# Optimization experiments

Hardware: AMD Instinct MI355X
Metric: run time of the kernel (lower is better)

Reference implementation:

```python
import jax, jax.numpy as jnp
import numpy as np

B, S, D_MODEL, D_HEAD = 8, 2048, 1024, 128
MAX_ROUNDS = 3
THRESH = 0.1
SCALE = 1.0 / np.sqrt(float(D_HEAD))


def setup_inputs() -> dict:
    key = jax.random.key(0)
    ks = jax.random.split(key, 12)

    def lin(k, out_d, in_d):
        # torch Linear weight layout [out, in], y = x @ W.T + b
        return (jax.random.normal(k, (out_d, in_d), jnp.float32) / np.sqrt(float(in_d))).astype(jnp.float32)

    thesis_w = lin(ks[3], D_HEAD, D_HEAD)
    return {
        "x": jax.random.normal(ks[0], (B, S, D_MODEL), jnp.float32),
        "wq": lin(ks[1], D_HEAD, D_MODEL),
        "wk": lin(ks[2], D_HEAD, D_MODEL),
        "wv": lin(ks[4], D_HEAD, D_MODEL),
        "thesis_w": thesis_w,  # antithesis weight is -thesis_w per __init__
        "thesis_b": 0.02 * jax.random.normal(ks[5], (D_HEAD,), jnp.float32),
        "anti_b": 0.02 * jax.random.normal(ks[6], (D_HEAD,), jnp.float32),
        "s_w1": lin(ks[7], D_HEAD, 3 * D_HEAD),
        "s_b1": jnp.zeros((D_HEAD,), jnp.float32),
        "s_w2": lin(ks[8], D_HEAD, D_HEAD),
        "s_b2": jnp.zeros((D_HEAD,), jnp.float32),
        "g_w": lin(ks[9], 1, 2 * D_HEAD),
        "g_b": jnp.zeros((1,), jnp.float32),
    }


def reference(x, wq, wk, wv, thesis_w, thesis_b, anti_b, s_w1, s_b1, s_w2, s_b2, g_w, g_b):
    # q/k/v projections (no bias)
    q = jnp.einsum("bsm,hm->bsh", x, wq)
    k = jnp.einsum("bsm,hm->bsh", x, wk)
    v = jnp.einsum("bsm,hm->bsh", x, wv)

    attn = jax.nn.softmax(jnp.einsum("bqh,bkh->bqk", q, k) * SCALE, axis=-1)
    # dropout is identity at eval time
    cur = jnp.einsum("bqk,bkh->bqh", attn, v)  # [B,S,Dh]

    # attn_weights and v never change across rounds, so thesis/antithesis are
    # round-invariant: compute the context projections once.
    context = cur
    thesis = context @ thesis_w.T + thesis_b
    anti = context @ (-thesis_w).T + anti_b  # antithesis weight = -thesis weight

    active = jnp.ones((B, S), dtype=bool)
    for _ in range(MAX_ROUNDS):
        # emulate `if not active_mask.any(): break` under jit
        any_active = jnp.any(active)
        am = active[..., None].astype(x.dtype)
        at, aa, ac = thesis * am, anti * am, cur * am

        h = jax.nn.relu(jnp.concatenate([at, aa, ac], axis=-1) @ s_w1.T + s_b1)
        synth = h @ s_w2.T + s_b2
        gate = jax.nn.sigmoid(jnp.concatenate([ac, synth], axis=-1) @ g_w.T + g_b)
        update = gate * (synth - ac) * 0.1
        new = cur + update  # applied to ALL tokens, matching original

        stable = jnp.linalg.norm(update, axis=-1) < THRESH  # new - cur == update
        cur = jnp.where(any_active, new, cur)
        active = jnp.where(any_active, active & ~stable, active)
    return cur
```

## Files before the change

### kernel.cpp

```cpp
#include <hip/hip_runtime.h>
#include <hip/hip_bf16.h>

#define B_   8
#define S_   2048
#define DM   1024
#define DH   128
#define BS_  16384
#define SCALE_  0.08838834764831845f
#define SCALE2_ 0.12751744f

typedef unsigned short u16;
typedef unsigned int   u32;
typedef _Float16 half8 __attribute__((ext_vector_type(8)));
typedef float    f32x4 __attribute__((ext_vector_type(4)));
typedef u32      u32x4 __attribute__((ext_vector_type(4)));

union H8 { u32x4 v; u32 u[4]; half8 h; };

__device__ __forceinline__ float bf2f(u16 u) {
    union { u32 i; float f; } w; w.i = ((u32)u) << 16; return w.f;
}
__device__ __forceinline__ void unpack8(uint4 v, float* f) {
    f[0] = bf2f(v.x & 0xffff); f[1] = bf2f(v.x >> 16);
    f[2] = bf2f(v.y & 0xffff); f[3] = bf2f(v.y >> 16);
    f[4] = bf2f(v.z & 0xffff); f[5] = bf2f(v.z >> 16);
    f[6] = bf2f(v.w & 0xffff); f[7] = bf2f(v.w >> 16);
}
__device__ __forceinline__ float ldE(const void* b, size_t i, int isbf16) {
    return isbf16 ? bf2f(((const u16*)b)[i]) : ((const float*)b)[i];
}
__device__ __forceinline__ void ld8(const void* b, size_t i, int isbf16, float* f) {
    if (isbf16) {
        unpack8(*(const uint4*)((const u16*)b + i), f);
    } else {
        float4 a = *(const float4*)((const float*)b + i);
        float4 c = *(const float4*)((const float*)b + i + 4);
        f[0] = a.x; f[1] = a.y; f[2] = a.z; f[3] = a.w;
        f[4] = c.x; f[5] = c.y; f[6] = c.z; f[7] = c.w;
    }
}
__device__ __forceinline__ u32 f2pk(float v) {
    _Float16 h = (_Float16)v;
    _Float16 l = (_Float16)(v - (float)h);
    union { _Float16 f; u16 u; } a, b; a.f = h; b.f = l;
    return ((u32)a.u << 16) | (u32)b.u;
}
__device__ __forceinline__ void split8(const float* f, u32x4& hi, u32x4& lo) {
    u32 H[8], L[8];
#pragma unroll
    for (int j = 0; j < 8; ++j) {
        _Float16 h = (_Float16)f[j];
        _Float16 l = (_Float16)(f[j] - (float)h);
        union { _Float16 x; u16 u; } a, b; a.x = h; b.x = l;
        H[j] = a.u; L[j] = b.u;
    }
    hi = (u32x4){H[0] | (H[1] << 16), H[2] | (H[3] << 16), H[4] | (H[5] << 16), H[6] | (H[7] << 16)};
    lo = (u32x4){L[0] | (L[1] << 16), L[2] | (L[3] << 16), L[4] | (L[5] << 16), L[6] | (L[7] << 16)};
}
__device__ __forceinline__ u32 permHI(u32 eB, u32 eA) { return __builtin_amdgcn_perm(eB, eA, 0x07060302u); }
__device__ __forceinline__ u32 permLO(u32 eB, u32 eA) { return __builtin_amdgcn_perm(eB, eA, 0x05040100u); }
__device__ __forceinline__ u16 f2h(float v) { union { _Float16 f; u16 u; } a; a.f = (_Float16)v; return a.u; }
__device__ __forceinline__ float h2f(u16 u) { union { _Float16 f; u16 u; } a; a.u = u; return (float)a.f; }

__global__ void init_kernel(const void* x, int* flag, int* active, int* counts) {
    int i = blockIdx.x * 256 + threadIdx.x;
    if (i < BS_) active[i] = 1;
    if (i < 4) counts[i] = (i == 0) ? BS_ : 0;
    if (i == 0) {
        const u16* w = (const u16*)x;
        int sane = 0;
        for (int t = 0; t < 256; ++t) {
            int e = (w[2 * t] >> 7) & 0xFF;
            if (e >= 100 && e <= 135) ++sane;
        }
        *flag = (sane >= 192) ? 1 : 0;
    }
}

__global__ __launch_bounds__(256) void prepack_w_kernel(
    const void* __restrict__ wq, const void* __restrict__ wk, const void* __restrict__ wv,
    const int* __restrict__ flag, u32x4* __restrict__ wpk)
{
    const int isb = *flag;
    const int gid = blockIdx.x * 256 + threadIdx.x;
    const int l  = gid & 63;
    const int t  = (gid >> 6) & 7;
    const int ks = (gid >> 9) & 31;
    const int z  = gid >> 14;
    const void* W = (z == 0) ? wq : (z == 1) ? wk : wv;
    const int row = 16 * t + (l & 15);
    const int k0  = ks * 32 + 8 * (l >> 4);
    float f[8];
    ld8(W, (size_t)row * DM + k0, isb, f);
    u32x4 hi, lo;
    split8(f, hi, lo);
    const size_t base = ((((size_t)z * 32 + ks) * 16) + 2 * t) * 64 + l;
    wpk[base]      = hi;
    wpk[base + 64] = lo;
}

__global__ __launch_bounds__(256) void qkv_kernel(
    const void* __restrict__ x, const u32x4* __restrict__ wpk,
    const int* __restrict__ flag, u32* __restrict__ qkv)
{
    const int isb = *flag;
    const int z = blockIdx.z;
    u32* out = qkv + (size_t)z * ((size_t)BS_ * DH);
    const int bx = blockIdx.x;
    const int m0 = ((bx & 7) * 32 + (bx >> 3)) * 64;
    const int tid = threadIdx.x;
    const int wave = tid >> 6, lane = tid & 63;
    const int qd = lane >> 4, c = lane & 15;

    __shared__ u32x4 WL[2][8][2][64];

    const u32x4* wz = wpk + (size_t)z * (32 * 16 * 64);
    const size_t arow = (size_t)(m0 + wave * 16 + c) * DM + 8 * qd;

#define STAGE_W(ks_, b_)                                                          \
    {                                                                             \
        const u32x4* _src = wz + ((size_t)(ks_) * 16 + 4 * wave) * 64 + lane;     \
        _Pragma("unroll")                                                         \
        for (int _j = 0; _j < 4; ++_j) {                                          \
            __builtin_amdgcn_global_load_lds(                                     \
                (const __attribute__((address_space(1))) u32*)(_src + _j * 64),   \
                (__attribute__((address_space(3))) u32*)&WL[b_][2 * wave + (_j >> 1)][_j & 1][0], \
                16, 0, 0);                                                        \
        }                                                                         \
    }

    float Ar[8], Arn[8];
    ld8(x, arow, isb, Ar);
    STAGE_W(0, 0);
    ld8(x, arow + 32, isb, Arn);
    __syncthreads();

    f32x4 acc[8] = {};

    for (int ks = 0; ks < 32; ++ks) {
        const int cb = ks & 1;
        if (ks + 1 < 32) STAGE_W(ks + 1, cb ^ 1);

        H8 Ah, Al;
        split8(Ar, Ah.v, Al.v);
#pragma unroll
        for (int t = 0; t < 8; ++t) {
            H8 bh, bl;
            bh.v = WL[cb][t][0][lane]; bl.v = WL[cb][t][1][lane];
            acc[t] = __builtin_amdgcn_mfma_f32_16x16x32_f16(Al.h, bh.h, acc[t], 0, 0, 0);
            acc[t] = __builtin_amdgcn_mfma_f32_16x16x32_f16(Ah.h, bl.h, acc[t], 0, 0, 0);
            acc[t] = __builtin_amdgcn_mfma_f32_16x16x32_f16(Ah.h, bh.h, acc[t], 0, 0, 0);
        }
#pragma unroll
        for (int j = 0; j < 8; ++j) Ar[j] = Arn[j];
        if (ks + 2 < 32) ld8(x, arow + (size_t)(ks + 2) * 32, isb, Arn);
        __syncthreads();
    }
#undef STAGE_W

#pragma unroll
    for (int r = 0; r < 4; ++r) {
        const int row = m0 + wave * 16 + qd * 4 + r;
        u32* op = out + (size_t)row * DH + c;
#pragma unroll
        for (int t = 0; t < 8; ++t) op[t * 16] = f2pk(acc[t][r]);
    }
}

template <bool WRITE_PARTIAL>
__device__ __forceinline__ void attn_body(
    const u32* qp, const u32* __restrict__ kp, const u32* __restrict__ vp,
    u16* outO, u16* outL, float* cur,
    int b, int q0, int kt0, int kt1, int part)
{
    const int tid = threadIdx.x;
    const int wave = tid >> 6, lane = tid & 63;
    const int qd = lane >> 4, c = lane & 15;

    __shared__ u32x4 KF[2][2][4][64];
    __shared__ u32x4 VF[2][8][64];
    __shared__ u16   PB[4][531];

    H8 Qh[4];
    {
        const u32* qr = qp + ((size_t)b * S_ + q0 + wave * 16 + c) * DH;
#pragma unroll
        for (int ks = 0; ks < 4; ++ks) {
            uint4 e0 = *(const uint4*)(qr + ks * 32 + qd * 8);
            uint4 e1 = *(const uint4*)(qr + ks * 32 + qd * 8 + 4);
            Qh[ks].u[0] = permHI(e0.y, e0.x); Qh[ks].u[1] = permHI(e0.w, e0.z);
            Qh[ks].u[2] = permHI(e1.y, e1.x); Qh[ks].u[3] = permHI(e1.w, e1.z);
        }
    }

    const int kKey = tid & 31, kD0 = (tid >> 5) * 16;
    const int vD = tid >> 1, vKg = (tid & 1) * 16;
    const int tK = (tid >> 4) & 1, cK = tid & 15;
    const int tV = tid >> 5,      cV = (tid >> 1) & 15;

    uint4 Kst[4]; u32 Vst[16];

    auto loadKV = [&](int kb) {
        const u32* kr = kp + ((size_t)b * S_ + kb * 32 + kKey) * DH + kD0;
#pragma unroll
        for (int j = 0; j < 4; ++j) Kst[j] = *(const uint4*)(kr + 4 * j);
        const u32* vc = vp + ((size_t)b * S_ + kb * 32 + vKg) * DH + vD;
#pragma unroll
        for (int j = 0; j < 16; ++j) Vst[j] = vc[(size_t)j * DH];
    };
    auto writeKV = [&](int wb) {
#pragma unroll
        for (int g = 0; g < 2; ++g) {
            const int dg = kD0 + 8 * g, ksK = dg >> 5, qK = (dg >> 3) & 3;
            KF[wb][tK][ksK][qK * 16 + cK] = (u32x4){
                permHI(Kst[2*g].y, Kst[2*g].x), permHI(Kst[2*g].w, Kst[2*g].z),
                permHI(Kst[2*g+1].y, Kst[2*g+1].x), permHI(Kst[2*g+1].w, Kst[2*g+1].z)};
        }
#pragma unroll
        for (int g = 0; g < 2; ++g) {
            const int qV = 2 * (tid & 1) + g;
            VF[wb][tV][qV * 16 + cV] = (u32x4){
                permHI(Vst[8*g+1], Vst[8*g+0]), permHI(Vst[8*g+3], Vst[8*g+2]),
                permHI(Vst[8*g+5], Vst[8*g+4]), permHI(Vst[8*g+7], Vst[8*g+6])};
        }
    };

    loadKV(kt0);
    writeKV(0);
    if (kt0 + 1 < kt1) loadKV(kt0 + 1);
    __syncthreads();

    f32x4 O[8] = {};
    float lsum[4] = {};

    for (int kt = kt0; kt < kt1; ++kt) {
        const int cb = (kt - kt0) & 1;

        f32x4 S0 = {}, S1 = {};
#pragma unroll
        for (int ks = 0; ks < 4; ++ks) {
            H8 kh;
            kh.v = KF[cb][0][ks][lane];
            S0 = __builtin_amdgcn_mfma_f32_16x16x32_f16(Qh[ks].h, kh.h, S0, 0, 0, 0);
            kh.v = KF[cb][1][ks][lane];
            S1 = __builtin_amdgcn_mfma_f32_16x16x32_f16(Qh[ks].h, kh.h, S1, 0, 0, 0);
        }

        u16* pw = PB[wave];
#pragma unroll
        for (int r = 0; r < 4; ++r) {
            float e0 = exp2f(fmaf(S0[r], SCALE2_, -4.0f));
            float e1 = exp2f(fmaf(S1[r], SCALE2_, -4.0f));
            lsum[r] += e0 + e1;
            pw[(4 * qd + r) * 33 + c]      = f2h(e0);
            pw[(4 * qd + r) * 33 + 16 + c] = f2h(e1);
        }

        u16 e[8];
#pragma unroll
        for (int j = 0; j < 8; ++j) e[j] = pw[c * 33 + 8 * qd + j];
        H8 Ph;
        Ph.u[0] = (u32)e[0] | ((u32)e[1] << 16);
        Ph.u[1] = (u32)e[2] | ((u32)e[3] << 16);
        Ph.u[2] = (u32)e[4] | ((u32)e[5] << 16);
        Ph.u[3] = (u32)e[6] | ((u32)e[7] << 16);

#pragma unroll
        for (int t = 0; t < 8; ++t) {
            H8 vh;
            vh.v = VF[cb][t][lane];
            O[t] = __builtin_amdgcn_mfma_f32_16x16x32_f16(Ph.h, vh.h, O[t], 0, 0, 0);
        }

        if (kt + 1 < kt1) {
            writeKV((kt + 1 - kt0) & 1);
            if (kt + 2 < kt1) loadKV(kt + 2);
        }
        __syncthreads();
    }

    if (WRITE_PARTIAL) {
        float lred[4];
#pragma unroll
        for (int r = 0; r < 4; ++r) {
            float l = lsum[r];
            l += __shfl_xor(l, 1); l += __shfl_xor(l, 2);
            l += __shfl_xor(l, 4); l += __shfl_xor(l, 8);
            lred[r] = l;
        }
        const size_t rb = (size_t)b * S_ + q0 + wave * 16 + 4 * qd;
        u16* Op = outO + (size_t)part * ((size_t)BS_ * DH);
#pragma unroll
        for (int t = 0; t < 8; ++t)
#pragma unroll
            for (int r = 0; r < 4; ++r)
                Op[(rb + r) * DH + t * 16 + c] = f2h(O[t][r]);
        if (c == 0) {
            u16* lp = outL + (size_t)part * BS_;
#pragma unroll
            for (int r = 0; r < 4; ++r) lp[rb + r] = f2h(lred[r]);
        }
    } else {
        float linv[4];
#pragma unroll
        for (int r = 0; r < 4; ++r) {
            float l = lsum[r];
            l += __shfl_xor(l, 1); l += __shfl_xor(l, 2);
            l += __shfl_xor(l, 4); l += __shfl_xor(l, 8);
            linv[r] = 1.0f / l;
        }
        const size_t rb = (size_t)b * S_ + q0 + wave * 16 + 4 * qd;
#pragma unroll
        for (int t = 0; t < 8; ++t)
#pragma unroll
            for (int r = 0; r < 4; ++r)
                cur[(rb + r) * DH + t * 16 + c] = O[t][r] * linv[r];
    }
}

__global__ __launch_bounds__(256) void attn_kernel(
    const u32* qp, const u32* __restrict__ kp, const u32* __restrict__ vp, float* cur)
{
    const int rid = blockIdx.x + 32 * blockIdx.y;
    attn_body<false>(qp, kp, vp, nullptr, nullptr, cur,
                     rid & 7, ((rid >> 3) & 31) * 64, 0, S_ / 32, 0);
}

__global__ __launch_bounds__(256) void attn_split_kernel(
    const u32* qp, const u32* __restrict__ kp, const u32* __restrict__ vp,
    u16* __restrict__ Opart, u16* __restrict__ lpart)
{
    const int rid = blockIdx.x + 32 * (blockIdx.y + 8 * blockIdx.z);
    const int b    = rid & 7;
    const int qx   = (rid >> 3) & 31;
    const int part = rid >> 8;
    const int quart = S_ / 128;
    attn_body<true>(qp, kp, vp, Opart, lpart, nullptr,
                    b, qx * 64, part * quart, (part + 1) * quart, part);
}

__global__ __launch_bounds__(256) void combine_kernel(
    const u16* __restrict__ Opart, const u16* __restrict__ lpart,
    float* __restrict__ cur)
{
    const size_t N1 = (size_t)BS_ * DH;
    const size_t i0 = ((size_t)blockIdx.x * 256 + threadIdx.x) * 16;
    const int row = (int)(i0 >> 7);
    const float lt = h2f(lpart[row]) + h2f(lpart[BS_ + row])
                   + h2f(lpart[2 * BS_ + row]) + h2f(lpart[3 * BS_ + row]);
    const float linv = 1.0f / lt;
    float acc[16] = {};
#pragma unroll
    for (int p = 0; p < 4; ++p) {
        const u16* op = Opart + (size_t)p * N1 + i0;
        uint4 v0 = *(const uint4*)op;
        uint4 v1 = *(const uint4*)(op + 8);
        const u32 w[8] = {v0.x, v0.y, v0.z, v0.w, v1.x, v1.y, v1.z, v1.w};
#pragma unroll
        for (int j = 0; j < 8; ++j) {
            acc[2 * j]     += h2f((u16)(w[j] & 0xffff));
            acc[2 * j + 1] += h2f((u16)(w[j] >> 16));
        }
    }
#pragma unroll
    for (int t = 0; t < 4; ++t)
        *(float4*)(cur + i0 + t * 4) = make_float4(
            acc[4*t] * linv, acc[4*t+1] * linv, acc[4*t+2] * linv, acc[4*t+3] * linv);
}

__global__ __launch_bounds__(256) void prepack_rw_kernel(
    const void* __restrict__ tw, const void* __restrict__ w1, const void* __restrict__ w2,
    const int* __restrict__ flag, u32x4* __restrict__ pk)
{
    const int isb = *flag;
    const int gid = blockIdx.x * 256 + threadIdx.x;
    const int l = gid & 63, t = (gid >> 6) & 7, ks = (gid >> 9) & 3, mat = gid >> 11;
    const int row = 16 * t + (l & 15);
    const int k0  = ks * 32 + 8 * (l >> 4);
    float f[8];
    if (mat == 0)      ld8(tw, (size_t)row * DH + k0, isb, f);
    else if (mat <= 3) ld8(w1, (size_t)row * 384 + (mat - 1) * 128 + k0, isb, f);
    else               ld8(w2, (size_t)row * DH + k0, isb, f);
    u32x4 hi, lo;
    split8(f, hi, lo);
    const size_t base = (((size_t)mat * 4 + ks) * 16 + 2 * t) * 64 + l;
    pk[base] = hi; pk[base + 64] = lo;
}

struct Afrag { H8 h[4], l[4]; };
__device__ __forceinline__ void splitA(const float (&A)[4][8], Afrag& F) {
#pragma unroll
    for (int ks = 0; ks < 4; ++ks) split8(A[ks], F.h[ks].v, F.l[ks].v);
}
__device__ __forceinline__ void gemm_wb(const Afrag& F, const u32x4 (*WB)[16][64],
                                        const int lane, f32x4 (&acc)[8])
{
#pragma unroll
    for (int ks = 0; ks < 4; ++ks) {
#pragma unroll
        for (int t = 0; t < 8; ++t) {
            H8 bh, bl;
            bh.v = WB[ks][2 * t][lane];
            bl.v = WB[ks][2 * t + 1][lane];
            acc[t] = __builtin_amdgcn_mfma_f32_16x16x32_f16(F.l[ks].h, bh.h, acc[t], 0, 0, 0);
            acc[t] = __builtin_amdgcn_mfma_f32_16x16x32_f16(F.h[ks].h, bl.h, acc[t], 0, 0, 0);
            acc[t] = __builtin_amdgcn_mfma_f32_16x16x32_f16(F.h[ks].h, bh.h, acc[t], 0, 0, 0);
        }
    }
}

__global__ __launch_bounds__(256) void round_kernel(
    const float* cur0, const float* curr,
    const u32x4* __restrict__ pk,
    const void* __restrict__ tb, const void* __restrict__ ab,
    const void* __restrict__ b1, const void* __restrict__ b2,
    const void* __restrict__ gw, const void* __restrict__ gb,
    const int* __restrict__ flag, int* active, int* counts, int r,
    float* cur_out, void* dout)
{
    const int isb = *flag;
    const int tok0 = blockIdx.x * 64;
    const int tid = threadIdx.x;
    const bool last = (dout != nullptr);

    if (counts[r] <= 0) {
        if (last) {
            for (int e = tid; e < 64 * DH; e += 256) {
                size_t idx = (size_t)tok0 * DH + e;
                float v = curr[idx];
                if (isb) ((__hip_bfloat16*)dout)[idx] = __float2bfloat16(v);
                else     ((float*)dout)[idx] = v;
            }
        }
        return;
    }

    const int wave = tid >> 6, lane = tid & 63;
    const int qd = lane >> 4, c = lane & 15;

    __shared__ u32x4 WB[4][16][64];
    __shared__ float T0S[64][132];
    __shared__ float HSS[64][132];
    __shared__ float actS[64], tbS[128], abS[128], b1S[128], b2S[128], gwS[256];
    __shared__ int blkcnt;

#define STAGE_RW(mat_)                                                             \
    {                                                                              \
        _Pragma("unroll")                                                          \
        for (int _j = 0; _j < 16; ++_j) {                                          \
            __builtin_amdgcn_global_load_lds(                                      \
                (const __attribute__((address_space(1))) u32*)(                    \
                    pk + (((size_t)(mat_) * 4 + wave) * 16 + _j) * 64 + lane),     \
                (__attribute__((address_space(3))) u32*)&WB[wave][_j][0],          \
                16, 0, 0);                                                         \
        }                                                                          \
    }

    STAGE_RW(0);
    if (tid < 64) actS[tid] = active[tok0 + tid] ? 1.0f : 0.0f;
    if (tid < 128) {
        tbS[tid] = ldE(tb, tid, isb); abS[tid] = ldE(ab, tid, isb);
        b1S[tid] = ldE(b1, tid, isb); b2S[tid] = ldE(b2, tid, isb);
    }
    gwS[tid] = ldE(gw, tid, isb);
    if (tid == 0) blkcnt = 0;
    const float gbf = ldE(gb, 0, isb);

    const int rowl = 16 * wave + c;
    const int hr   = 16 * wave + 4 * qd;

    float A1[4][8];
    {
        const float* cr = cur0 + (size_t)(tok0 + rowl) * DH;
#pragma unroll
        for (int ks = 0; ks < 4; ++ks) {
            *(float4*)&A1[ks][0] = *(const float4*)(cr + ks * 32 + 8 * qd);
            *(float4*)&A1[ks][4] = *(const float4*)(cr + ks * 32 + 8 * qd + 4);
        }
    }
    Afrag FA; splitA(A1, FA);
    __syncthreads();

    {
        f32x4 acc[8] = {};
        gemm_wb(FA, WB, lane, acc);
#pragma unroll
        for (int t = 0; t < 8; ++t)
#pragma unroll
            for (int rr = 0; rr < 4; ++rr)
                T0S[hr + rr][16 * t + c] = acc[t][rr];
    }
    __syncthreads();
    STAGE_RW(1);

    f32x4 acc1[8] = {};
    const float am_r = actS[rowl];
    {
        float Ac[4][8];
#pragma unroll
        for (int ks = 0; ks < 4; ++ks)
#pragma unroll
            for (int j = 0; j < 8; ++j) {
                const int k = ks * 32 + 8 * qd + j;
                Ac[ks][j] = (T0S[rowl][k] + tbS[k]) * am_r;
            }
        Afrag FC; splitA(Ac, FC);
        __syncthreads();
        gemm_wb(FC, WB, lane, acc1);
    }
    __syncthreads();
    STAGE_RW(2);
    {
        float Ac[4][8];
#pragma unroll
        for (int ks = 0; ks < 4; ++ks)
#pragma unroll
            for (int j = 0; j < 8; ++j) {
                const int k = ks * 32 + 8 * qd + j;
                Ac[ks][j] = (abS[k] - T0S[rowl][k]) * am_r;
            }
        Afrag FC; splitA(Ac, FC);
        __syncthreads();
        gemm_wb(FC, WB, lane, acc1);
    }
    __syncthreads();
    STAGE_RW(3);
    {
        float Ac[4][8];
        const float* cr = curr + (size_t)(tok0 + rowl) * DH;
#pragma unroll
        for (int ks = 0; ks < 4; ++ks) {
            float4 a0 = *(const float4*)(cr + ks * 32 + 8 * qd);
            float4 a1 = *(const float4*)(cr + ks * 32 + 8 * qd + 4);
            Ac[ks][0] = a0.x * am_r; Ac[ks][1] = a0.y * am_r;
            Ac[ks][2] = a0.z * am_r; Ac[ks][3] = a0.w * am_r;
            Ac[ks][4] = a1.x * am_r; Ac[ks][5] = a1.y * am_r;
            Ac[ks][6] = a1.z * am_r; Ac[ks][7] = a1.w * am_r;
        }
        Afrag FC; splitA(Ac, FC);
        __syncthreads();
        gemm_wb(FC, WB, lane, acc1);
    }
#pragma unroll
    for (int t = 0; t < 8; ++t)
#pragma unroll
        for (int rr = 0; rr < 4; ++rr)
            HSS[hr + rr][16 * t + c] = fmaxf(acc1[t][rr] + b1S[16 * t + c], 0.0f);
    __syncthreads();
    STAGE_RW(4);
    {
        float Ac[4][8];
#pragma unroll
        for (int ks = 0; ks < 4; ++ks) {
            const float* hp = &HSS[rowl][ks * 32 + 8 * qd];
            *(float4*)&Ac[ks][0] = *(const float4*)hp;
            *(float4*)&Ac[ks][4] = *(const float4*)(hp + 4);
        }
        Afrag FC; splitA(Ac, FC);
        __syncthreads();
        f32x4 acc2[8] = {};
        gemm_wb(FC, WB, lane, acc2);
#pragma unroll
        for (int t = 0; t < 8; ++t)
#pragma unroll
            for (int rr = 0; rr < 4; ++rr)
                T0S[hr + rr][16 * t + c] = acc2[t][rr] + b2S[16 * t + c];
    }
    __syncthreads();

    const int tok = tid >> 2, d0 = (tid & 3) * 32;
    const float am = actS[tok];
    const float* cp = curr + (size_t)(tok0 + tok) * DH + d0;
    float cv[32];
#pragma unroll
    for (int t = 0; t < 8; ++t) {
        float4 vv = *(const float4*)(cp + t * 4);
        cv[t * 4] = vv.x; cv[t * 4 + 1] = vv.y; cv[t * 4 + 2] = vv.z; cv[t * 4 + 3] = vv.w;
    }
    const float* srow = &T0S[tok][d0];
    float gp = 0.0f;
#pragma unroll
    for (int e = 0; e < 32; ++e)
        gp += cv[e] * am * gwS[d0 + e] + srow[e] * gwS[128 + d0 + e];
    gp += __shfl_xor(gp, 1, 4);
    gp += __shfl_xor(gp, 2, 4);
    const float gate = 1.0f / (1.0f + __expf(-(gp + gbf)));
    float ss = 0.0f; float up[32];
#pragma unroll
    for (int e = 0; e < 32; ++e) {
        float u = gate * (srow[e] - cv[e] * am) * 0.1f;
        up[e] = u; ss += u * u;
    }
    ss += __shfl_xor(ss, 1, 4);
    ss += __shfl_xor(ss, 2, 4);
    const bool stable = sqrtf(ss) < 0.1f;

    if (last) {
        size_t off = (size_t)(tok0 + tok) * DH + d0;
        if (isb) {
            __hip_bfloat16* op = (__hip_bfloat16*)dout + off;
#pragma unroll
            for (int e = 0; e < 32; ++e) op[e] = __float2bfloat16(cv[e] + up[e]);
        } else {
            float* op = (float*)dout + off;
#pragma unroll
            for (int t = 0; t < 8; ++t)
                *(float4*)(op + t * 4) = make_float4(cv[t * 4] + up[t * 4], cv[t * 4 + 1] + up[t * 4 + 1],
                                                     cv[t * 4 + 2] + up[t * 4 + 2], cv[t * 4 + 3] + up[t * 4 + 3]);
        }
    } else {
        float* op = cur_out + (size_t)(tok0 + tok) * DH + d0;
#pragma unroll
        for (int t = 0; t < 8; ++t)
            *(float4*)(op + t * 4) = make_float4(cv[t * 4] + up[t * 4], cv[t * 4 + 1] + up[t * 4 + 1],
                                                 cv[t * 4 + 2] + up[t * 4 + 2], cv[t * 4 + 3] + up[t * 4 + 3]);
    }
    const int newact = (am > 0.0f && !stable) ? 1 : 0;
    if ((tid & 3) == 0) {
        active[tok0 + tok] = newact;
        if (newact) atomicAdd(&blkcnt, 1);
    }
    __syncthreads();
    if (tid == 0 && blkcnt > 0) atomicAdd(&counts[r + 1], blkcnt);
#undef STAGE_RW
}

extern "C" void kernel_launch(void* const* d_in, const int* in_sizes, int n_in,
                              void* d_out, int out_size, void* d_ws, size_t ws_size,
                              hipStream_t stream) {
    const void* x  = d_in[0];
    const void* wq = d_in[1];
    const void* wk = d_in[2];
    const void* wv = d_in[3];
    const void* tw = d_in[4];
    const void* tb = d_in[5];
    const void* ab = d_in[6];
    const void* w1 = d_in[7];
    const void* b1 = d_in[8];
    const void* w2 = d_in[9];
    const void* b2 = d_in[10];
    const void* gw = d_in[11];
    const void* gb = d_in[12];

    u32* ws = (u32*)d_ws;
    const size_t N1 = (size_t)BS_ * DH;
    u32* qp = ws;
    u32* kp = ws + N1;
    u32* vp = ws + 2 * N1;
    int* active = (int*)(ws + 3 * N1);
    int* counts = active + BS_;
    int* flag   = counts + 4;
    float* cur0  = (float*)qp;
    float* cur_r = (float*)kp;
    u16* Opart16 = (u16*)(ws + 3 * N1 + 32768);
    u16* lpart16 = (u16*)(ws + 5 * N1 + 32768);
    const bool big_ws = ws_size >= (size_t)42300000;
    u32x4* wpk = (u32x4*)(ws + 3 * N1 + 32768);
    u32x4* pkRW = (u32x4*)vp;

    init_kernel<<<dim3(BS_ / 256), 256, 0, stream>>>(x, flag, active, counts);
    prepack_w_kernel<<<dim3(192), 256, 0, stream>>>(wq, wk, wv, flag, wpk);
    qkv_kernel<<<dim3(BS_ / 64, 1, 3), 256, 0, stream>>>(x, wpk, flag, qp);
    if (big_ws) {
        attn_split_kernel<<<dim3(S_ / 64, B_, 4), 256, 0, stream>>>(qp, kp, vp, Opart16, lpart16);
        combine_kernel<<<dim3(512), 256, 0, stream>>>(Opart16, lpart16, cur0);
    } else {
        attn_kernel<<<dim3(S_ / 64, B_), 256, 0, stream>>>(qp, kp, vp, cur0);
    }
    prepack_rw_kernel<<<dim3(40), 256, 0, stream>>>(tw, w1, w2, flag, pkRW);
    round_kernel<<<dim3(BS_ / 64), 256, 0, stream>>>(
        cur0, cur0, pkRW, tb, ab, b1, b2, gw, gb, flag, active, counts, 0, cur_r, nullptr);
    round_kernel<<<dim3(BS_ / 64), 256, 0, stream>>>(
        cur0, cur_r, pkRW, tb, ab, b1, b2, gw, gb, flag, active, counts, 1, cur_r, nullptr);
    round_kernel<<<dim3(BS_ / 64), 256, 0, stream>>>(
        cur0, cur_r, pkRW, tb, ab, b1, b2, gw, gb, flag, active, counts, 2, cur_r, d_out);
}
```

Measured before the change: 283.6 us.

## Emit K/V in MFMA fragment layout and drop split-precision terms for bf16 inputs

The QKV kernel now writes K and V as half-precision MFMA-ready fragments, staged through shared memory, so the attention kernel reads them straight from global memory with no LDS staging, double buffering or per-tile barriers. When inputs are detected as bf16, the QKV GEMM uses only the high fp16 part, one MFMA instead of three, and the round kernel skips the hi*lo correction term. This cuts MFMA work and LDS traffic but lowers precision for K/V (fp16 only) and, on the bf16 path, for the projections. Attention now relies on cache behaviour instead of explicit LDS reuse.

```diff
diff --git a/kernel.cpp b/kernel.cpp
--- a/kernel.cpp
+++ b/kernel.cpp
@@ -57,8 +57,16 @@
     hi = (u32x4){H[0] | (H[1] << 16), H[2] | (H[3] << 16), H[4] | (H[5] << 16), H[6] | (H[7] << 16)};
     lo = (u32x4){L[0] | (L[1] << 16), L[2] | (L[3] << 16), L[4] | (L[5] << 16), L[6] | (L[7] << 16)};
 }
+__device__ __forceinline__ void cvt8hi(const float* f, u32x4& hi) {
+    u32 H[8];
+#pragma unroll
+    for (int j = 0; j < 8; ++j) {
+        union { _Float16 x; u16 u; } a; a.x = (_Float16)f[j];
+        H[j] = a.u;
+    }
+    hi = (u32x4){H[0] | (H[1] << 16), H[2] | (H[3] << 16), H[4] | (H[5] << 16), H[6] | (H[7] << 16)};
+}
 __device__ __forceinline__ u32 permHI(u32 eB, u32 eA) { return __builtin_amdgcn_perm(eB, eA, 0x07060302u); }
-__device__ __forceinline__ u32 permLO(u32 eB, u32 eA) { return __builtin_amdgcn_perm(eB, eA, 0x05040100u); }
 __device__ __forceinline__ u16 f2h(float v) { union { _Float16 f; u16 u; } a; a.f = (_Float16)v; return a.u; }
 __device__ __forceinline__ float h2f(u16 u) { union { _Float16 f; u16 u; } a; a.u = u; return (float)a.f; }
 
@@ -101,11 +109,11 @@
 
 __global__ __launch_bounds__(256) void qkv_kernel(
     const void* __restrict__ x, const u32x4* __restrict__ wpk,
-    const int* __restrict__ flag, u32* __restrict__ qkv)
+    const int* __restrict__ flag, u32* __restrict__ qout,
+    u32x4* __restrict__ kfrag, u32x4* __restrict__ vfrag)
 {
     const int isb = *flag;
     const int z = blockIdx.z;
-    u32* out = qkv + (size_t)z * ((size_t)BS_ * DH);
     const int bx = blockIdx.x;
     const int m0 = ((bx & 7) * 32 + (bx >> 3)) * 64;
     const int tid = threadIdx.x;
@@ -113,6 +121,7 @@
     const int qd = lane >> 4, c = lane & 15;
 
     __shared__ u32x4 WL[2][8][2][64];
+    __shared__ u16 TS[64][136];
 
     const u32x4* wz = wpk + (size_t)z * (32 * 16 * 64);
     const size_t arow = (size_t)(m0 + wave * 16 + c) * DM + 8 * qd;
@@ -141,15 +150,26 @@
         const int cb = ks & 1;
         if (ks + 1 < 32) STAGE_W(ks + 1, cb ^ 1);
 
-        H8 Ah, Al;
-        split8(Ar, Ah.v, Al.v);
-#pragma unroll
-        for (int t = 0; t < 8; ++t) {
-            H8 bh, bl;
-            bh.v = WL[cb][t][0][lane]; bl.v = WL[cb][t][1][lane];
-            acc[t] = __builtin_amdgcn_mfma_f32_16x16x32_f16(Al.h, bh.h, acc[t], 0, 0, 0);
-            acc[t] = __builtin_amdgcn_mfma_f32_16x16x32_f16(Ah.h, bl.h, acc[t], 0, 0, 0);
-            acc[t] = __builtin_amdgcn_mfma_f32_16x16x32_f16(Ah.h, bh.h, acc[t], 0, 0, 0);
+        if (isb) {
+            H8 Ah;
+            cvt8hi(Ar, Ah.v);
+#pragma unroll
+            for (int t = 0; t < 8; ++t) {
+                H8 bh;
+                bh.v = WL[cb][t][0][lane];
+                acc[t] = __builtin_amdgcn_mfma_f32_16x16x32_f16(Ah.h, bh.h, acc[t], 0, 0, 0);
+            }
+        } else {
+            H8 Ah, Al;
+            split8(Ar, Ah.v, Al.v);
+#pragma unroll
+            for (int t = 0; t < 8; ++t) {
+                H8 bh, bl;
+                bh.v = WL[cb][t][0][lane]; bl.v = WL[cb][t][1][lane];
+                acc[t] = __builtin_amdgcn_mfma_f32_16x16x32_f16(Al.h, bh.h, acc[t], 0, 0, 0);
+                acc[t] = __builtin_amdgcn_mfma_f32_16x16x32_f16(Ah.h, bl.h, acc[t], 0, 0, 0);
+                acc[t] = __builtin_amdgcn_mfma_f32_16x16x32_f16(Ah.h, bh.h, acc[t], 0, 0, 0);
+            }
         }
 #pragma unroll
         for (int j = 0; j < 8; ++j) Ar[j] = Arn[j];
@@ -158,18 +178,54 @@
     }
 #undef STAGE_W
 
-#pragma unroll
-    for (int r = 0; r < 4; ++r) {
-        const int row = m0 + wave * 16 + qd * 4 + r;
-        u32* op = out + (size_t)row * DH + c;
-#pragma unroll
-        for (int t = 0; t < 8; ++t) op[t * 16] = f2pk(acc[t][r]);
+    if (z == 0) {
+#pragma unroll
+        for (int r = 0; r < 4; ++r) {
+            const int row = m0 + wave * 16 + qd * 4 + r;
+            u32* op = qout + (size_t)row * DH + c;
+#pragma unroll
+            for (int t = 0; t < 8; ++t) op[t * 16] = f2pk(acc[t][r]);
+        }
+    } else {
+#pragma unroll
+        for (int t = 0; t < 8; ++t)
+#pragma unroll
+            for (int r = 0; r < 4; ++r)
+                TS[wave * 16 + qd * 4 + r][16 * t + c] = f2h(acc[t][r]);
+        __syncthreads();
+        if (z == 1) {
+#pragma unroll
+            for (int i = 0; i < 4; ++i) {
+                const int f = tid + 256 * i;
+                const int lf = f & 63, ks = (f >> 6) & 3, sub = f >> 8;
+                const int key = sub * 16 + (lf & 15);
+                const int d0  = ks * 32 + 8 * (lf >> 4);
+                u32 w[4];
+#pragma unroll
+                for (int q = 0; q < 4; ++q)
+                    w[q] = (u32)TS[key][d0 + 2 * q] | ((u32)TS[key][d0 + 2 * q + 1] << 16);
+                kfrag[((size_t)(m0 / 16 + sub) * 4 + ks) * 64 + lf] = (u32x4){w[0], w[1], w[2], w[3]};
+            }
+        } else {
+#pragma unroll
+            for (int i = 0; i < 4; ++i) {
+                const int f = tid + 256 * i;
+                const int lf = f & 63, t = (f >> 6) & 7, sub = f >> 9;
+                const int kb2 = sub * 32 + 8 * (lf >> 4);
+                const int dh  = 16 * t + (lf & 15);
+                u32 w[4];
+#pragma unroll
+                for (int q = 0; q < 4; ++q)
+                    w[q] = (u32)TS[kb2 + 2 * q][dh] | ((u32)TS[kb2 + 2 * q + 1][dh] << 16);
+                vfrag[((size_t)(m0 / 32 + sub) * 8 + t) * 64 + lf] = (u32x4){w[0], w[1], w[2], w[3]};
+            }
+        }
     }
 }
 
 template <bool WRITE_PARTIAL>
 __device__ __forceinline__ void attn_body(
-    const u32* qp, const u32* __restrict__ kp, const u32* __restrict__ vp,
+    const u32* qp, const u32x4* __restrict__ kfrag, const u32x4* __restrict__ vfrag,
     u16* outO, u16* outL, float* cur,
     int b, int q0, int kt0, int kt1, int part)
 {
@@ -177,9 +233,7 @@
     const int wave = tid >> 6, lane = tid & 63;
     const int qd = lane >> 4, c = lane & 15;
 
-    __shared__ u32x4 KF[2][2][4][64];
-    __shared__ u32x4 VF[2][8][64];
-    __shared__ u16   PB[4][531];
+    __shared__ u16 PB[4][531];
 
     H8 Qh[4];
     {
@@ -193,56 +247,23 @@
         }
     }
 
-    const int kKey = tid & 31, kD0 = (tid >> 5) * 16;
-    const int vD = tid >> 1, vKg = (tid & 1) * 16;
-    const int tK = (tid >> 4) & 1, cK = tid & 15;
-    const int tV = tid >> 5,      cV = (tid >> 1) & 15;
-
-    uint4 Kst[4]; u32 Vst[16];
-
-    auto loadKV = [&](int kb) {
-        const u32* kr = kp + ((size_t)b * S_ + kb * 32 + kKey) * DH + kD0;
-#pragma unroll
-        for (int j = 0; j < 4; ++j) Kst[j] = *(const uint4*)(kr + 4 * j);
-        const u32* vc = vp + ((size_t)b * S_ + kb * 32 + vKg) * DH + vD;
-#pragma unroll
-        for (int j = 0; j < 16; ++j) Vst[j] = vc[(size_t)j * DH];
-    };
-    auto writeKV = [&](int wb) {
-#pragma unroll
-        for (int g = 0; g < 2; ++g) {
-            const int dg = kD0 + 8 * g, ksK = dg >> 5, qK = (dg >> 3) & 3;
-            KF[wb][tK][ksK][qK * 16 + cK] = (u32x4){
-                permHI(Kst[2*g].y, Kst[2*g].x), permHI(Kst[2*g].w, Kst[2*g].z),
-                permHI(Kst[2*g+1].y, Kst[2*g+1].x), permHI(Kst[2*g+1].w, Kst[2*g+1].z)};
-        }
-#pragma unroll
-        for (int g = 0; g < 2; ++g) {
-            const int qV = 2 * (tid & 1) + g;
-            VF[wb][tV][qV * 16 + cV] = (u32x4){
-                permHI(Vst[8*g+1], Vst[8*g+0]), permHI(Vst[8*g+3], Vst[8*g+2]),
-                permHI(Vst[8*g+5], Vst[8*g+4]), permHI(Vst[8*g+7], Vst[8*g+6])};
-        }
-    };
-
-    loadKV(kt0);
-    writeKV(0);
-    if (kt0 + 1 < kt1) loadKV(kt0 + 1);
-    __syncthreads();
-
     f32x4 O[8] = {};
     float lsum[4] = {};
 
+    const u32x4* kb0 = kfrag + (size_t)b * 128 * 256;
+    const u32x4* vb0 = vfrag + (size_t)b * 64 * 512;
+
     for (int kt = kt0; kt < kt1; ++kt) {
-        const int cb = (kt - kt0) & 1;
+        const u32x4* kf = kb0 + (size_t)kt * 512;
+        const u32x4* vf = vb0 + (size_t)kt * 512;
 
         f32x4 S0 = {}, S1 = {};
 #pragma unroll
         for (int ks = 0; ks < 4; ++ks) {
             H8 kh;
-            kh.v = KF[cb][0][ks][lane];
+            kh.v = kf[ks * 64 + lane];
             S0 = __builtin_amdgcn_mfma_f32_16x16x32_f16(Qh[ks].h, kh.h, S0, 0, 0, 0);
-            kh.v = KF[cb][1][ks][lane];
+            kh.v = kf[256 + ks * 64 + lane];
             S1 = __builtin_amdgcn_mfma_f32_16x16x32_f16(Qh[ks].h, kh.h, S1, 0, 0, 0);
         }
 
@@ -268,15 +289,9 @@
 #pragma unroll
         for (int t = 0; t < 8; ++t) {
             H8 vh;
-            vh.v = VF[cb][t][lane];
+            vh.v = vf[t * 64 + lane];
             O[t] = __builtin_amdgcn_mfma_f32_16x16x32_f16(Ph.h, vh.h, O[t], 0, 0, 0);
         }
-
-        if (kt + 1 < kt1) {
-            writeKV((kt + 1 - kt0) & 1);
-            if (kt + 2 < kt1) loadKV(kt + 2);
-        }
-        __syncthreads();
     }
 
     if (WRITE_PARTIAL) {
@@ -319,15 +334,15 @@
 }
 
 __global__ __launch_bounds__(256) void attn_kernel(
-    const u32* qp, const u32* __restrict__ kp, const u32* __restrict__ vp, float* cur)
+    const u32* qp, const u32x4* __restrict__ kfrag, const u32x4* __restrict__ vfrag, float* cur)
 {
     const int rid = blockIdx.x + 32 * blockIdx.y;
-    attn_body<false>(qp, kp, vp, nullptr, nullptr, cur,
+    attn_body<false>(qp, kfrag, vfrag, nullptr, nullptr, cur,
                      rid & 7, ((rid >> 3) & 31) * 64, 0, S_ / 32, 0);
 }
 
 __global__ __launch_bounds__(256) void attn_split_kernel(
-    const u32* qp, const u32* __restrict__ kp, const u32* __restrict__ vp,
+    const u32* qp, const u32x4* __restrict__ kfrag, const u32x4* __restrict__ vfrag,
     u16* __restrict__ Opart, u16* __restrict__ lpart)
 {
     const int rid = blockIdx.x + 32 * (blockIdx.y + 8 * blockIdx.z);
@@ -335,7 +350,7 @@
     const int qx   = (rid >> 3) & 31;
     const int part = rid >> 8;
     const int quart = S_ / 128;
-    attn_body<true>(qp, kp, vp, Opart, lpart, nullptr,
+    attn_body<true>(qp, kfrag, vfrag, Opart, lpart, nullptr,
                     b, qx * 64, part * quart, (part + 1) * quart, part);
 }
 
@@ -393,7 +408,7 @@
     for (int ks = 0; ks < 4; ++ks) split8(A[ks], F.h[ks].v, F.l[ks].v);
 }
 __device__ __forceinline__ void gemm_wb(const Afrag& F, const u32x4 (*WB)[16][64],
-                                        const int lane, f32x4 (&acc)[8])
+                                        const int lane, const int isb, f32x4 (&acc)[8])
 {
 #pragma unroll
     for (int ks = 0; ks < 4; ++ks) {
@@ -403,7 +418,8 @@
             bh.v = WB[ks][2 * t][lane];
             bl.v = WB[ks][2 * t + 1][lane];
             acc[t] = __builtin_amdgcn_mfma_f32_16x16x32_f16(F.l[ks].h, bh.h, acc[t], 0, 0, 0);
-            acc[t] = __builtin_amdgcn_mfma_f32_16x16x32_f16(F.h[ks].h, bl.h, acc[t], 0, 0, 0);
+            if (!isb)
+                acc[t] = __builtin_amdgcn_mfma_f32_16x16x32_f16(F.h[ks].h, bl.h, acc[t], 0, 0, 0);
             acc[t] = __builtin_amdgcn_mfma_f32_16x16x32_f16(F.h[ks].h, bh.h, acc[t], 0, 0, 0);
         }
     }
@@ -483,7 +499,7 @@
 
     {
         f32x4 acc[8] = {};
-        gemm_wb(FA, WB, lane, acc);
+        gemm_wb(FA, WB, lane, isb, acc);
 #pragma unroll
         for (int t = 0; t < 8; ++t)
 #pragma unroll
@@ -506,7 +522,7 @@
             }
         Afrag FC; splitA(Ac, FC);
         __syncthreads();
-        gemm_wb(FC, WB, lane, acc1);
+        gemm_wb(FC, WB, lane, isb, acc1);
     }
     __syncthreads();
     STAGE_RW(2);
@@ -521,7 +537,7 @@
             }
         Afrag FC; splitA(Ac, FC);
         __syncthreads();
-        gemm_wb(FC, WB, lane, acc1);
+        gemm_wb(FC, WB, lane, isb, acc1);
     }
     __syncthreads();
     STAGE_RW(3);
@@ -539,7 +555,7 @@
         }
         Afrag FC; splitA(Ac, FC);
         __syncthreads();
-        gemm_wb(FC, WB, lane, acc1);
+        gemm_wb(FC, WB, lane, isb, acc1);
     }
 #pragma unroll
     for (int t = 0; t < 8; ++t)
@@ -559,7 +575,7 @@
         Afrag FC; splitA(Ac, FC);
         __syncthreads();
         f32x4 acc2[8] = {};
-        gemm_wb(FC, WB, lane, acc2);
+        gemm_wb(FC, WB, lane, isb, acc2);
 #pragma unroll
         for (int t = 0; t < 8; ++t)
 #pragma unroll
@@ -657,15 +673,17 @@
     const bool big_ws = ws_size >= (size_t)42300000;
     u32x4* wpk = (u32x4*)(ws + 3 * N1 + 32768);
     u32x4* pkRW = (u32x4*)vp;
+    u32x4* kfragP = (u32x4*)kp;
+    u32x4* vfragP = (u32x4*)vp;
 
     init_kernel<<<dim3(BS_ / 256), 256, 0, stream>>>(x, flag, active, counts);
     prepack_w_kernel<<<dim3(192), 256, 0, stream>>>(wq, wk, wv, flag, wpk);
-    qkv_kernel<<<dim3(BS_ / 64, 1, 3), 256, 0, stream>>>(x, wpk, flag, qp);
+    qkv_kernel<<<dim3(BS_ / 64, 1, 3), 256, 0, stream>>>(x, wpk, flag, qp, kfragP, vfragP);
     if (big_ws) {
-        attn_split_kernel<<<dim3(S_ / 64, B_, 4), 256, 0, stream>>>(qp, kp, vp, Opart16, lpart16);
+        attn_split_kernel<<<dim3(S_ / 64, B_, 4), 256, 0, stream>>>(qp, kfragP, vfragP, Opart16, lpart16);
         combine_kernel<<<dim3(512), 256, 0, stream>>>(Opart16, lpart16, cur0);
     } else {
-        attn_kernel<<<dim3(S_ / 64, B_), 256, 0, stream>>>(qp, kp, vp, cur0);
+        attn_kernel<<<dim3(S_ / 64, B_), 256, 0, stream>>>(qp, kfragP, vfragP, cur0);
     }
     prepack_rw_kernel<<<dim3(40), 256, 0, stream>>>(tw, w1, w2, flag, pkRW);
     round_kernel<<<dim3(BS_ / 64), 256, 0, stream>>>(
```

Result: faster. 275.8 us (-2.7%).
